# Kernel tuning notes

Measured on AMD Instinct MI355X. Metric: run time of the kernel, lower is better.

The kernel has to match this reference:

```python
import jax, jax.numpy as jnp
import numpy as np

B, L, CIN, COUT = 8, 2048, 1024, 1024


def setup_inputs() -> dict:
    key = jax.random.key(0)
    ks = jax.random.split(key, 13)
    s_in = 1.0 / np.sqrt(CIN)
    s_out = 1.0 / np.sqrt(COUT)
    return {
        "query": jax.random.normal(ks[0], (B, L, CIN), jnp.float32),
        "key": jax.random.normal(ks[1], (B, L, CIN), jnp.float32),
        "value": jax.random.normal(ks[2], (B, L, CIN), jnp.float32),
        "Wq": jax.random.uniform(ks[3], (COUT, CIN), jnp.float32, -s_in, s_in),
        "bq": jax.random.uniform(ks[4], (COUT,), jnp.float32, -s_in, s_in),
        "Wk": jax.random.uniform(ks[5], (COUT, CIN), jnp.float32, -s_in, s_in),
        "bk": jax.random.uniform(ks[6], (COUT,), jnp.float32, -s_in, s_in),
        "Wv": jax.random.uniform(ks[7], (COUT, CIN), jnp.float32, -s_in, s_in),
        "bv": jax.random.uniform(ks[8], (COUT,), jnp.float32, -s_in, s_in),
        "fcq_w": jax.random.uniform(ks[9], (1, COUT), jnp.float32, -s_out, s_out),
        "fcq_b": jax.random.uniform(ks[10], (1,), jnp.float32, -s_out, s_out),
        "fck_w": jax.random.uniform(ks[11], (1, COUT), jnp.float32, -s_out, s_out),
        "fck_b": jax.random.uniform(ks[12], (1,), jnp.float32, -s_out, s_out),
    }


def reference(query, key, value, Wq, bq, Wk, bk, Wv, bv, fcq_w, fcq_b, fck_w, fck_b):
    # Linear projections (torch Linear: x @ W^T + b)
    w_query = jnp.einsum('blc,oc->blo', query, Wq) + bq   # [B, Lq, COUT]
    w_key = jnp.einsum('blc,oc->blo', key, Wk) + bk       # [B, Lk, COUT]
    w_value = jnp.einsum('blc,oc->blo', value, Wv) + bv   # [B, Lk, COUT]
    # Scalar scores per position, then outer-sum -> [B, Lq, Lk]
    fc_query = jnp.einsum('blo,xo->blx', w_query, fcq_w) + fcq_b  # [B, Lq, 1]
    fc_key = jnp.einsum('blo,xo->blx', w_key, fck_w) + fck_b      # [B, Lk, 1]
    attns = fc_query + jnp.swapaxes(fc_key, 1, 2)                 # [B, Lq, Lk]
    attns = jax.nn.softmax(attns, axis=-1)
    # dropout p=0.0 (eval) -> identity
    outputs = jnp.einsum('bqk,bkd->bqd', attns, w_value)          # [B, Lq, COUT]
    # note: original applies activation to attns after bmm but discards it
    return outputs
```

## Files before the change

### kernel.cpp

```cpp
#include <hip/hip_runtime.h>

#define CIN  1024
#define COUT 1024
#define LB   2048
#define BB   8


__global__ void k_u(const float* __restrict__ Wk, const float* __restrict__ fckw,
                    float* __restrict__ u) {
    int tid = threadIdx.x;
    int bc = blockIdx.x & 3;
    int oc = blockIdx.x >> 2;
    int c = bc * 256 + tid;
    int o0 = oc * 128;
    float acc = 0.f;
    #pragma unroll 4
    for (int o = o0; o < o0 + 128; ++o)
        acc += fckw[o] * Wk[(size_t)o * CIN + c];
    atomicAdd(&u[c], acc);
}

__global__ void k_scores(const float* __restrict__ key, const float* __restrict__ u,
                         float* __restrict__ s) {
    __shared__ float su[CIN];
    int tid = threadIdx.x;
    ((float4*)su)[tid] = ((const float4*)u)[tid];
    __syncthreads();
    int wave = tid >> 6, lane = tid & 63;
    int r = blockIdx.x * 4 + wave;
    const float4* row = (const float4*)(key + (size_t)r * CIN);
    const float4* su4 = (const float4*)su;
    float acc = 0.f;
    #pragma unroll
    for (int j = 0; j < 4; ++j) {
        float4 a = row[lane + j * 64];
        float4 b = su4[lane + j * 64];
        acc += a.x * b.x + a.y * b.y + a.z * b.z + a.w * b.w;
    }
    #pragma unroll
    for (int off = 32; off; off >>= 1) acc += __shfl_down(acc, off, 64);
    if (lane == 0) s[r] = acc;
}

__global__ void k_softmax(const float* __restrict__ s, float* __restrict__ p) {
    __shared__ float red[256];
    int b = blockIdx.x, t = threadIdx.x;
    const float* sb = s + (size_t)b * LB;
    float v[8];
    float m = -1e30f;
    #pragma unroll
    for (int j = 0; j < 8; ++j) { v[j] = sb[t + j * 256]; m = fmaxf(m, v[j]); }
    red[t] = m; __syncthreads();
    for (int o = 128; o; o >>= 1) { if (t < o) red[t] = fmaxf(red[t], red[t + o]); __syncthreads(); }
    m = red[0]; __syncthreads();
    float sum = 0.f;
    #pragma unroll
    for (int j = 0; j < 8; ++j) { v[j] = expf(v[j] - m); sum += v[j]; }
    red[t] = sum; __syncthreads();
    for (int o = 128; o; o >>= 1) { if (t < o) red[t] += red[t + o]; __syncthreads(); }
    float inv = 1.f / red[0];
    float* pb = p + (size_t)b * LB;
    #pragma unroll
    for (int j = 0; j < 8; ++j) pb[t + j * 256] = v[j] * inv;
}

__global__ void k_vbar(const float* __restrict__ value, const float* __restrict__ p,
                       float* __restrict__ vbar) {
    __shared__ float pl[64];
    int t = threadIdx.x;
    int blk = blockIdx.x;
    int b  = blk >> 7;
    int cc = (blk >> 5) & 3;
    int kc = blk & 31;
    int c  = cc * 256 + t;
    int k0 = kc * 64;
    if (t < 64) pl[t] = p[(size_t)b * LB + k0 + t];
    __syncthreads();
    const float* vb = value + ((size_t)b * LB + k0) * CIN + c;
    float acc = 0.f;
    #pragma unroll 4
    for (int i = 0; i < 64; ++i) acc += pl[i] * vb[(size_t)i * CIN];
    atomicAdd(&vbar[(size_t)b * CIN + c], acc);
}

__global__ void k_orow(const float* __restrict__ Wv, const float* __restrict__ bv,
                       const float* __restrict__ vbar, float* __restrict__ orow) {
    __shared__ float sv[CIN];
    int tid = threadIdx.x;
    int r0 = blockIdx.x * 4;
    int b = r0 >> 10;
    ((float4*)sv)[tid] = ((const float4*)(vbar + (size_t)b * CIN))[tid];
    __syncthreads();
    int wave = tid >> 6, lane = tid & 63;
    int r = r0 + wave;
    int d = r & 1023;
    const float4* row = (const float4*)(Wv + (size_t)d * CIN);
    const float4* sv4 = (const float4*)sv;
    float acc = 0.f;
    #pragma unroll
    for (int j = 0; j < 4; ++j) {
        float4 a = row[lane + j * 64];
        float4 v = sv4[lane + j * 64];
        acc += a.x * v.x + a.y * v.y + a.z * v.z + a.w * v.w;
    }
    #pragma unroll
    for (int off = 32; off; off >>= 1) acc += __shfl_down(acc, off, 64);
    if (lane == 0) orow[r] = acc + bv[d];
}

__global__ void k_bcast(const float* __restrict__ orow, float* __restrict__ out) {
    const float4* o4 = (const float4*)orow;
    float4* out4 = (float4*)out;
    const size_t total = (size_t)BB * LB * (COUT / 4);
    for (size_t f = (size_t)blockIdx.x * blockDim.x + threadIdx.x; f < total;
         f += (size_t)gridDim.x * blockDim.x) {
        int d4  = (int)(f & 255);
        int row = (int)(f >> 8);
        int b   = row >> 11;
        out4[f] = o4[b * 256 + d4];
    }
}

extern "C" void kernel_launch(void* const* d_in, const int* in_sizes, int n_in,
                              void* d_out, int out_size, void* d_ws, size_t ws_size,
                              hipStream_t stream) {
    const float* key   = (const float*)d_in[1];
    const float* value = (const float*)d_in[2];
    const float* Wk    = (const float*)d_in[5];
    const float* Wv    = (const float*)d_in[7];
    const float* bv    = (const float*)d_in[8];
    const float* fckw  = (const float*)d_in[11];

    float* ws   = (float*)d_ws;
    float* u    = ws;
    float* s    = ws + 1024;
    float* p    = ws + 17408;
    float* vbar = ws + 33792;
    float* orow = ws + 41984;
    float* out  = (float*)d_out;

    hipMemsetAsync(ws, 0, 50176 * sizeof(float), stream);

    hipLaunchKernelGGL(k_u,       dim3(32),   dim3(256), 0, stream, Wk, fckw, u);
    hipLaunchKernelGGL(k_scores,  dim3(4096), dim3(256), 0, stream, key, u, s);
    hipLaunchKernelGGL(k_softmax, dim3(8),    dim3(256), 0, stream, s, p);
    hipLaunchKernelGGL(k_vbar,    dim3(1024), dim3(256), 0, stream, value, p, vbar);
    hipLaunchKernelGGL(k_orow,    dim3(2048), dim3(256), 0, stream, Wv, bv, vbar, orow);
    hipLaunchKernelGGL(k_bcast,   dim3(2048), dim3(256), 0, stream, orow, out);
}
```

Before: 250.2 us.

## Vectorize reduction kernels, fold vbar zeroing into softmax, shrink memset

Several kernels are rewritten together. k_u and k_vbar now load float4 and get a new split of work across blocks. Softmax uses wave shuffles with fast exp and also zeroes vbar, so the memset only has to clear u. k_bcast switches from a grid-stride loop to fixed 8 rows per block. The goal is fewer memory transactions and less launch and memset overhead in a pipeline dominated by memory bandwidth. The costs are more atomics per block in k_vbar and slightly less accurate exp.

```diff
diff --git a/kernel.cpp b/kernel.cpp
--- a/kernel.cpp
+++ b/kernel.cpp
@@ -6,22 +6,44 @@
 #define BB   8
 
 
-__global__ void k_u(const float* __restrict__ Wk, const float* __restrict__ fckw,
-                    float* __restrict__ u) {
-    int tid = threadIdx.x;
-    int bc = blockIdx.x & 3;
+__global__ __launch_bounds__(256) void k_u(const float* __restrict__ Wk,
+                                           const float* __restrict__ fckw,
+                                           float* __restrict__ u) {
+    __shared__ float4 red[256];
+    const float4* Wk4 = (const float4*)Wk;
+    int t = threadIdx.x;
+    int cc = blockIdx.x & 3;
     int oc = blockIdx.x >> 2;
-    int c = bc * 256 + tid;
-    int o0 = oc * 128;
-    float acc = 0.f;
-    #pragma unroll 4
-    for (int o = o0; o < o0 + 128; ++o)
-        acc += fckw[o] * Wk[(size_t)o * CIN + c];
-    atomicAdd(&u[c], acc);
+    int c4 = cc * 64 + (t & 63);
+    int w  = t >> 6;
+    float4 acc = make_float4(0.f, 0.f, 0.f, 0.f);
+    #pragma unroll
+    for (int j = 0; j < 16; ++j) {
+        int o = oc * 64 + w + j * 4;
+        float f = fckw[o];
+        float4 a = Wk4[(size_t)o * 256 + c4];
+        acc.x += f * a.x; acc.y += f * a.y; acc.z += f * a.z; acc.w += f * a.w;
+    }
+    red[t] = acc;
+    __syncthreads();
+    if (t < 64) {
+        float4 a = red[t], b = red[t + 64], c = red[t + 128], d = red[t + 192];
+        float4 s;
+        s.x = a.x + b.x + c.x + d.x;
+        s.y = a.y + b.y + c.y + d.y;
+        s.z = a.z + b.z + c.z + d.z;
+        s.w = a.w + b.w + c.w + d.w;
+        float* up = u + (size_t)cc * 256 + t * 4;
+        atomicAdd(up + 0, s.x);
+        atomicAdd(up + 1, s.y);
+        atomicAdd(up + 2, s.z);
+        atomicAdd(up + 3, s.w);
+    }
 }
 
-__global__ void k_scores(const float* __restrict__ key, const float* __restrict__ u,
-                         float* __restrict__ s) {
+__global__ __launch_bounds__(256) void k_scores(const float* __restrict__ key,
+                                                const float* __restrict__ u,
+                                                float* __restrict__ s) {
     __shared__ float su[CIN];
     int tid = threadIdx.x;
     ((float4*)su)[tid] = ((const float4*)u)[tid];
@@ -42,49 +64,67 @@
     if (lane == 0) s[r] = acc;
 }
 
-__global__ void k_softmax(const float* __restrict__ s, float* __restrict__ p) {
-    __shared__ float red[256];
+__global__ __launch_bounds__(256) void k_softmax(const float* __restrict__ s,
+                                                 float* __restrict__ p,
+                                                 float* __restrict__ vbar) {
+    __shared__ float wred[4];
     int b = blockIdx.x, t = threadIdx.x;
-    const float* sb = s + (size_t)b * LB;
-    float v[8];
-    float m = -1e30f;
+    int wave = t >> 6, lane = t & 63;
+    const float4* s4 = (const float4*)(s + (size_t)b * LB);
+    float4 v0 = s4[t], v1 = s4[t + 256];
+    float m = fmaxf(fmaxf(fmaxf(v0.x, v0.y), fmaxf(v0.z, v0.w)),
+                    fmaxf(fmaxf(v1.x, v1.y), fmaxf(v1.z, v1.w)));
     #pragma unroll
-    for (int j = 0; j < 8; ++j) { v[j] = sb[t + j * 256]; m = fmaxf(m, v[j]); }
-    red[t] = m; __syncthreads();
-    for (int o = 128; o; o >>= 1) { if (t < o) red[t] = fmaxf(red[t], red[t + o]); __syncthreads(); }
-    m = red[0]; __syncthreads();
-    float sum = 0.f;
+    for (int off = 32; off; off >>= 1) m = fmaxf(m, __shfl_down(m, off, 64));
+    if (lane == 0) wred[wave] = m;
+    __syncthreads();
+    m = fmaxf(fmaxf(wred[0], wred[1]), fmaxf(wred[2], wred[3]));
+    __syncthreads();
+    v0.x = __expf(v0.x - m); v0.y = __expf(v0.y - m);
+    v0.z = __expf(v0.z - m); v0.w = __expf(v0.w - m);
+    v1.x = __expf(v1.x - m); v1.y = __expf(v1.y - m);
+    v1.z = __expf(v1.z - m); v1.w = __expf(v1.w - m);
+    float sum = v0.x + v0.y + v0.z + v0.w + v1.x + v1.y + v1.z + v1.w;
     #pragma unroll
-    for (int j = 0; j < 8; ++j) { v[j] = expf(v[j] - m); sum += v[j]; }
-    red[t] = sum; __syncthreads();
-    for (int o = 128; o; o >>= 1) { if (t < o) red[t] += red[t + o]; __syncthreads(); }
-    float inv = 1.f / red[0];
-    float* pb = p + (size_t)b * LB;
-    #pragma unroll
-    for (int j = 0; j < 8; ++j) pb[t + j * 256] = v[j] * inv;
+    for (int off = 32; off; off >>= 1) sum += __shfl_down(sum, off, 64);
+    if (lane == 0) wred[wave] = sum;
+    __syncthreads();
+    float inv = 1.f / (wred[0] + wred[1] + wred[2] + wred[3]);
+    v0.x *= inv; v0.y *= inv; v0.z *= inv; v0.w *= inv;
+    v1.x *= inv; v1.y *= inv; v1.z *= inv; v1.w *= inv;
+    float4* p4 = (float4*)(p + (size_t)b * LB);
+    p4[t] = v0; p4[t + 256] = v1;
+    ((float4*)(vbar + (size_t)b * CIN))[t] = make_float4(0.f, 0.f, 0.f, 0.f);
 }
 
-__global__ void k_vbar(const float* __restrict__ value, const float* __restrict__ p,
-                       float* __restrict__ vbar) {
-    __shared__ float pl[64];
+__global__ __launch_bounds__(256) void k_vbar(const float* __restrict__ value,
+                                              const float* __restrict__ p,
+                                              float* __restrict__ vbar) {
+    __shared__ float pl[32];
     int t = threadIdx.x;
-    int blk = blockIdx.x;
-    int b  = blk >> 7;
-    int cc = (blk >> 5) & 3;
-    int kc = blk & 31;
-    int c  = cc * 256 + t;
-    int k0 = kc * 64;
-    if (t < 64) pl[t] = p[(size_t)b * LB + k0 + t];
+    int b  = blockIdx.x >> 6;
+    int k0 = (blockIdx.x & 63) * 32;
+    if (t < 32) pl[t] = p[(size_t)b * LB + k0 + t];
     __syncthreads();
-    const float* vb = value + ((size_t)b * LB + k0) * CIN + c;
-    float acc = 0.f;
-    #pragma unroll 4
-    for (int i = 0; i < 64; ++i) acc += pl[i] * vb[(size_t)i * CIN];
-    atomicAdd(&vbar[(size_t)b * CIN + c], acc);
+    const float4* v4 = (const float4*)value + ((size_t)b * LB + k0) * 256 + t;
+    float4 acc = make_float4(0.f, 0.f, 0.f, 0.f);
+    #pragma unroll 8
+    for (int k = 0; k < 32; ++k) {
+        float pw = pl[k];
+        float4 a = v4[(size_t)k * 256];
+        acc.x += pw * a.x; acc.y += pw * a.y; acc.z += pw * a.z; acc.w += pw * a.w;
+    }
+    float* vp = vbar + (size_t)b * CIN + t * 4;
+    atomicAdd(vp + 0, acc.x);
+    atomicAdd(vp + 1, acc.y);
+    atomicAdd(vp + 2, acc.z);
+    atomicAdd(vp + 3, acc.w);
 }
 
-__global__ void k_orow(const float* __restrict__ Wv, const float* __restrict__ bv,
-                       const float* __restrict__ vbar, float* __restrict__ orow) {
+__global__ __launch_bounds__(256) void k_orow(const float* __restrict__ Wv,
+                                              const float* __restrict__ bv,
+                                              const float* __restrict__ vbar,
+                                              float* __restrict__ orow) {
     __shared__ float sv[CIN];
     int tid = threadIdx.x;
     int r0 = blockIdx.x * 4;
@@ -108,17 +148,16 @@
     if (lane == 0) orow[r] = acc + bv[d];
 }
 
-__global__ void k_bcast(const float* __restrict__ orow, float* __restrict__ out) {
-    const float4* o4 = (const float4*)orow;
+__global__ __launch_bounds__(256) void k_bcast(const float* __restrict__ orow,
+                                               float* __restrict__ out) {
+    int t = threadIdx.x;
+    int b  = blockIdx.x >> 8;
+    int q0 = (blockIdx.x & 255) * 8;
+    float4 val = ((const float4*)orow)[b * 256 + t];
     float4* out4 = (float4*)out;
-    const size_t total = (size_t)BB * LB * (COUT / 4);
-    for (size_t f = (size_t)blockIdx.x * blockDim.x + threadIdx.x; f < total;
-         f += (size_t)gridDim.x * blockDim.x) {
-        int d4  = (int)(f & 255);
-        int row = (int)(f >> 8);
-        int b   = row >> 11;
-        out4[f] = o4[b * 256 + d4];
-    }
+    #pragma unroll
+    for (int j = 0; j < 8; ++j)
+        out4[((size_t)b * LB + q0 + j) * 256 + t] = val;
 }
 
 extern "C" void kernel_launch(void* const* d_in, const int* in_sizes, int n_in,
@@ -139,12 +178,12 @@
     float* orow = ws + 41984;
     float* out  = (float*)d_out;
 
-    hipMemsetAsync(ws, 0, 50176 * sizeof(float), stream);
+    hipMemsetAsync(u, 0, 1024 * sizeof(float), stream);
 
-    hipLaunchKernelGGL(k_u,       dim3(32),   dim3(256), 0, stream, Wk, fckw, u);
+    hipLaunchKernelGGL(k_u,       dim3(64),   dim3(256), 0, stream, Wk, fckw, u);
     hipLaunchKernelGGL(k_scores,  dim3(4096), dim3(256), 0, stream, key, u, s);
-    hipLaunchKernelGGL(k_softmax, dim3(8),    dim3(256), 0, stream, s, p);
-    hipLaunchKernelGGL(k_vbar,    dim3(1024), dim3(256), 0, stream, value, p, vbar);
+    hipLaunchKernelGGL(k_softmax, dim3(8),    dim3(256), 0, stream, s, p, vbar);
+    hipLaunchKernelGGL(k_vbar,    dim3(512),  dim3(256), 0, stream, value, p, vbar);
     hipLaunchKernelGGL(k_orow,    dim3(2048), dim3(256), 0, stream, Wv, bv, vbar, orow);
     hipLaunchKernelGGL(k_bcast,   dim3(2048), dim3(256), 0, stream, orow, out);
 }
```

Result: faster. 242.4 us (-3.1%).
